# Optimization experiments

Hardware: AMD Instinct MI355X
Metric: run time of the kernel (lower is better)

## Reference

```python
import jax, jax.numpy as jnp
import numpy as np

MIN_NORM = 1e-15

# ---- Poincare-ball (c=1) Mobius algebra, matching geoopt pmath ----

def expmap0(u):
    n = jnp.maximum(jnp.linalg.norm(u, axis=-1, keepdims=True), MIN_NORM)
    return jnp.tanh(n) * u / n

def mobius_add(x, y):
    x2 = jnp.sum(x * x, -1, keepdims=True)
    y2 = jnp.sum(y * y, -1, keepdims=True)
    xy = jnp.sum(x * y, -1, keepdims=True)
    num = (1 + 2 * xy + y2) * x + (1 - x2) * y
    den = 1 + 2 * xy + x2 * y2
    return num / jnp.maximum(den, MIN_NORM)

def mobius_matvec(M, x):
    # M: [H, D, D], x: [B, H, D] -> [B, H, D]  (one matvec per ball)
    x_norm = jnp.maximum(jnp.linalg.norm(x, axis=-1, keepdims=True), MIN_NORM)
    mx = jnp.einsum('hij,bhj->bhi', M, x)
    mx_norm = jnp.maximum(jnp.linalg.norm(mx, axis=-1, keepdims=True), MIN_NORM)
    scale = jnp.tanh(mx_norm / x_norm * jnp.arctanh(jnp.minimum(x_norm, 1 - 1e-7)))
    res = scale * mx / mx_norm
    zero_mx = jnp.all(mx == 0, axis=-1, keepdims=True)
    return jnp.where(zero_mx, jnp.zeros_like(res), res)

def hyper_rnn(x_seq, W, U, b):
    # x_seq: [B, S, H, D] -> encodings [B, S, H, D]
    B, S, H, D = x_seq.shape
    h0 = jnp.zeros((B, H, D), x_seq.dtype)
    def step(h, x_t):
        wh = mobius_matvec(W, h)
        ux = mobius_matvec(U, x_t)
        h_new = mobius_add(mobius_add(wh, ux), b)
        return h_new, h_new
    _, out = jax.lax.scan(step, h0, jnp.swapaxes(x_seq, 0, 1))
    return jnp.swapaxes(out, 0, 1)

def poinc_dist_all_labels(enc, label_embed):
    # enc: [B,S,H,D], label_embed: [L,H,D] -> dist [B,S,L,H]
    # dist(x,y) = arccosh(1 + 2||x-y||^2 / ((1-||x||^2)(1-||y||^2)))  (c=1)
    a = jnp.sum(enc * enc, -1)                 # [B,S,H]
    lb = jnp.sum(label_embed * label_embed, -1)  # [L,H]
    dot = jnp.einsum('bshd,lhd->bslh', enc, label_embed)  # [B,S,L,H]
    c2 = jnp.maximum(a[:, :, None, :] + lb[None, None, :, :] - 2 * dot, 0.0)
    denom = (1 - a)[:, :, None, :] * (1 - lb)[None, None, :, :]
    arg = 1 + 2 * c2 / jnp.maximum(denom, MIN_NORM)
    return jnp.arccosh(jnp.maximum(arg, 1 + 1e-7))

def setup_inputs() -> dict:
    key = jax.random.key(0)
    ks = jax.random.split(key, 10)
    B, S, V, L, H, D = 32, 256, 30000, 1024, 4, 64
    k = 1.0 / np.sqrt(D)
    x = jax.random.randint(ks[0], (B, S), 0, V, dtype=jnp.int64) if jax.config.jax_enable_x64 else jax.random.randint(ks[0], (B, S), 0, V, dtype=jnp.int32)
    word_embed = expmap0(0.05 * jax.random.normal(ks[1], (V, H, D), jnp.float32))
    label_embed = expmap0(0.05 * jax.random.normal(ks[2], (L, H, D), jnp.float32))
    W = jax.random.uniform(ks[3], (H, D, D), jnp.float32, -k, k)
    U = jax.random.uniform(ks[4], (H, D, D), jnp.float32, -k, k)
    b = expmap0(0.01 * jax.random.normal(ks[5], (H, D), jnp.float32))
    k1 = 1.0 / np.sqrt(S)
    w1 = jax.random.uniform(ks[6], (S // 2, S), jnp.float32, -k1, k1)
    b1 = jax.random.uniform(ks[7], (S // 2,), jnp.float32, -k1, k1)
    k2 = 1.0 / np.sqrt(S // 2)
    w2 = jax.random.uniform(ks[8], (1, S // 2), jnp.float32, -k2, k2)
    b2 = jax.random.uniform(ks[9], (1,), jnp.float32, -k2, k2)
    return {"x": x, "word_embed": word_embed, "label_embed": label_embed,
            "W": W, "U": U, "b": b, "w1": w1, "b1": b1, "w2": w2, "b2": b2}

def reference(x, word_embed, label_embed, W, U, b, w1, b1, w2, b2):
    we = word_embed[x]                         # [B,S,H,D]
    enc = hyper_rnn(we, W, U, b)               # [B,S,H,D]
    dist = poinc_dist_all_labels(enc, label_embed)  # [B,S,L,H]
    interaction = jnp.transpose(dist.sum(-1), (0, 2, 1))  # [B,L,S]
    h1 = jax.nn.relu(jnp.einsum('bls,fs->blf', interaction, w1) + b1)
    out = (jnp.einsum('blf,of->blo', h1, w2) + b2).squeeze(-1)  # [B,L]
    return out
```

## Files before the change

### kernel.cpp

```cpp
#include <hip/hip_runtime.h>
#include <math.h>

#define MIN_NORM 1e-15f


__device__ __forceinline__ float frcp(float x){ return __builtin_amdgcn_rcpf(x); }
__device__ __forceinline__ float fsqrt(float x){ return __builtin_amdgcn_sqrtf(x); }
__device__ __forceinline__ float fast_atanh(float x){
  return 0.5f * __logf((1.f + x) * frcp(1.f - x));
}
__device__ __forceinline__ float fast_tanh(float y){
  float e = __expf(-2.f * y);
  return (1.f - e) * frcp(1.f + e);
}
__device__ __forceinline__ float rdlane(float v, int l){
  return __int_as_float(__builtin_amdgcn_readlane(__float_as_int(v), l));
}

#define DPPADD(v, ctrl) \
  v += __int_as_float(__builtin_amdgcn_update_dpp(0, __float_as_int(v), ctrl, 0xf, 0xf, false));

__device__ __forceinline__ float wred_b(float v){
  DPPADD(v,0x111) DPPADD(v,0x112) DPPADD(v,0x114) DPPADD(v,0x118)
  DPPADD(v,0x142) DPPADD(v,0x143)
  return __int_as_float(__builtin_amdgcn_readlane(__float_as_int(v), 63));
}
__device__ __forceinline__ void wred3_b(float& v0, float& v1, float& v2){
  DPPADD(v0,0x111) DPPADD(v1,0x111) DPPADD(v2,0x111)
  DPPADD(v0,0x112) DPPADD(v1,0x112) DPPADD(v2,0x112)
  DPPADD(v0,0x114) DPPADD(v1,0x114) DPPADD(v2,0x114)
  DPPADD(v0,0x118) DPPADD(v1,0x118) DPPADD(v2,0x118)
  DPPADD(v0,0x142) DPPADD(v1,0x142) DPPADD(v2,0x142)
  DPPADD(v0,0x143) DPPADD(v1,0x143) DPPADD(v2,0x143)
  v0 = __int_as_float(__builtin_amdgcn_readlane(__float_as_int(v0), 63));
  v1 = __int_as_float(__builtin_amdgcn_readlane(__float_as_int(v1), 63));
  v2 = __int_as_float(__builtin_amdgcn_readlane(__float_as_int(v2), 63));
}

__device__ __forceinline__ float wred(float v){
#pragma unroll
  for(int o=32;o;o>>=1) v += __shfl_xor(v, o, 64);
  return v;
}

#define LDS_FENCE() asm volatile("s_waitcnt lgkmcnt(0)" ::: "memory")

#define MATVEC64(RES, WROW, HSARR) {                                     \
  float a0=0.f,a1=0.f,a2=0.f,a3=0.f,a4=0.f,a5=0.f,a6=0.f,a7=0.f;         \
  _Pragma("unroll")                                                      \
  for(int j=0;j<64;j+=8){                                                \
    float4 h4 = *(const float4*)(&(HSARR)[j]);                           \
    float4 h5 = *(const float4*)(&(HSARR)[j+4]);                         \
    a0 = fmaf((WROW)[j  ], h4.x, a0); a1 = fmaf((WROW)[j+1], h4.y, a1);  \
    a2 = fmaf((WROW)[j+2], h4.z, a2); a3 = fmaf((WROW)[j+3], h4.w, a3);  \
    a4 = fmaf((WROW)[j+4], h5.x, a4); a5 = fmaf((WROW)[j+5], h5.y, a5);  \
    a6 = fmaf((WROW)[j+6], h5.z, a6); a7 = fmaf((WROW)[j+7], h5.w, a7);  \
  }                                                                      \
  RES = ((a0+a1)+(a2+a3)) + ((a4+a5)+(a6+a7));                           \
}

#define MATVEC_RL(RES, WROW, MV) {                                       \
  float a0=0.f,a1=0.f,a2=0.f,a3=0.f,a4=0.f,a5=0.f,a6=0.f,a7=0.f;         \
  _Pragma("unroll")                                                      \
  for(int j=0;j<64;j+=8){                                                \
    a0 = fmaf(rdlane(MV,j  ), (WROW)[j  ], a0);                          \
    a1 = fmaf(rdlane(MV,j+1), (WROW)[j+1], a1);                          \
    a2 = fmaf(rdlane(MV,j+2), (WROW)[j+2], a2);                          \
    a3 = fmaf(rdlane(MV,j+3), (WROW)[j+3], a3);                          \
    a4 = fmaf(rdlane(MV,j+4), (WROW)[j+4], a4);                          \
    a5 = fmaf(rdlane(MV,j+5), (WROW)[j+5], a5);                          \
    a6 = fmaf(rdlane(MV,j+6), (WROW)[j+6], a6);                          \
    a7 = fmaf(rdlane(MV,j+7), (WROW)[j+7], a7);                          \
  }                                                                      \
  RES = ((a0+a1)+(a2+a3)) + ((a4+a5)+(a6+a7));                           \
}

__global__ __launch_bounds__(256) void k_ux(const int* __restrict__ x,
    const float* __restrict__ wemb, const float* __restrict__ U,
    const float* __restrict__ Wm, const float* __restrict__ bvec,
    float* __restrict__ ux, float* __restrict__ wux,
    float* __restrict__ uxn2, float* __restrict__ uxb){
  __shared__ __align__(16) float xs[4][64];
  const int wv = threadIdx.x >> 6, lane = threadIdx.x & 63;
  const int bid = blockIdx.x*4 + wv;
  const int h = bid & 3;
  const int bs = bid >> 2;
  const int v = x[bs];
  float xi = wemb[(size_t)v*256 + h*64 + lane];
  const float bi = bvec[h*64 + lane];
  xs[wv][lane] = xi;
  LDS_FENCE();
  float mx; MATVEC64(mx, U + h*4096 + lane*64, xs[wv]);
  float t0 = xi*xi, t1 = mx*mx, t2 = mx*bi;
  wred3_b(t0, t1, t2);
  float xn  = fmaxf(fsqrt(t0), MIN_NORM);
  float mxn = fmaxf(fsqrt(t1), MIN_NORM);
  float scale = fast_tanh(mxn*frcp(xn) * fast_atanh(fminf(xn, 1.f-1e-7f)));
  float sm = scale * frcp(mxn);
  float uxv = sm * mx;
  ux[(size_t)bid*64 + lane] = uxv;
  if(lane==0){
    uxn2[bid] = (t1 > 0.f) ? scale*scale : 0.f;
    uxb[bid]  = sm * t2;
  }
  xs[wv][lane] = uxv;
  LDS_FENCE();
  float wuv; MATVEC64(wuv, Wm + h*4096 + lane*64, xs[wv]);
  wux[(size_t)bid*64 + lane] = wuv;
}

#define RNN_STEP(S, USLOT, WUSLOT, Y2V, UBV) {                           \
  const float U_ = USLOT, WU_ = WUSLOT;                                  \
  const float Y2_ = (Y2V), UB_ = (UBV);                                  \
  if((S) < 254){                                   \
    USLOT  = uxp  [(size_t)((S)+2)*256 + lane];                          \
    WUSLOT = wuxp [(size_t)((S)+2)*256 + lane];                          \
  }                                                                      \
  float p0 = m*m, p1 = m*U_, p2 = m*bi;                                  \
  wred3_b(p0, p1, p2);                                                   \
  float r_; MATVEC_RL(r_, wrow, m);           \
  float xn  = fmaxf(fsqrt(hh), MIN_NORM);                                \
  float mxn = fmaxf(fsqrt(p0), MIN_NORM);                                \
  float at  = fast_atanh(fminf(xn, 1.f-1e-7f));                          \
  float scale = fast_tanh(mxn*frcp(xn)*at);                              \
  float sm  = scale*frcp(mxn);                                           \
  float wx2 = (p0 > 0.f) ? scale*scale : 0.f;                            \
  float xy  = sm*p1;                                                     \
  float A   = 1.f + 2.f*xy + Y2_;                                        \
  float Bc  = 1.f - wx2;                                                 \
  float iden = frcp(fmaxf(1.f + 2.f*xy + wx2*Y2_, MIN_NORM));            \
  float c1 = A*sm*iden, c2 = Bc*iden;                                    \
  float zz = (A*A*wx2 + 2.f*A*Bc*xy + Bc*Bc*Y2_)*iden*iden;              \
  float zb = (A*sm*p2 + Bc*UB_)*iden;                                    \
  float A2 = 1.f + 2.f*zb + bn2v;                                        \
  float B2 = 1.f - zz;                                                   \
  float iden2 = frcp(fmaxf(1.f + 2.f*zb + zz*bn2v, MIN_NORM));           \
  float e  = A2*iden2, ga = B2*iden2;                                    \
  float al = e*c1, be = e*c2;                                            \
  encp[(size_t)(S)*256 + lane] = fmaf(al, m, fmaf(be, U_, ga*bi));       \
  hh = fmaxf(e*e*zz + 2.f*e*ga*zb + ga*ga*bn2v, 0.f);                    \
  m  = fmaf(al, r_, fmaf(be, WU_, ga*wb));                               \
}

#define RNN_BLOCK(BLK, Y2R, UBR)                                         \
  for(int i=0;i<64;i+=2){                                                \
    RNN_STEP((BLK)*64+i,   uA, wuA, rdlane(Y2R, i),   rdlane(UBR, i));   \
    RNN_STEP((BLK)*64+i+1, uB, wuB, rdlane(Y2R, i+1), rdlane(UBR, i+1)); \
  }

__global__ __launch_bounds__(64) void k_rnn(const float* __restrict__ W,
    const float* __restrict__ bvec, const float* __restrict__ ux,
    const float* __restrict__ wux, const float* __restrict__ uxn2,
    const float* __restrict__ uxb, float* __restrict__ enc){
  const int b = blockIdx.x >> 2, h = blockIdx.x & 3;
  const int lane = threadIdx.x;
  float wrow[64];
  const float* Wp = W + h*4096 + lane*64;
#pragma unroll
  for(int j=0;j<64;j+=4){
    float4 w4 = *(const float4*)(Wp + j);
    wrow[j]=w4.x; wrow[j+1]=w4.y; wrow[j+2]=w4.z; wrow[j+3]=w4.w;
  }
  const float bi = bvec[h*64 + lane];
  const float bn2v = wred_b(bi*bi);
  float wb; MATVEC_RL(wb, wrow, bi);
  const float* uxp   = ux   + (size_t)b*65536 + h*64;
  const float* wuxp  = wux  + (size_t)b*65536 + h*64;
  const float* uxn2p = uxn2 + (size_t)b*1024  + h;
  const float* uxbp  = uxb  + (size_t)b*1024  + h;
  float* encp        = enc  + (size_t)b*65536 + h*64;
  float y2r0 = uxn2p[(      lane)*4], ubr0 = uxbp[(      lane)*4];
  float y2r1 = uxn2p[( 64 + lane)*4], ubr1 = uxbp[( 64 + lane)*4];
  float y2r2 = uxn2p[(128 + lane)*4], ubr2 = uxbp[(128 + lane)*4];
  float y2r3 = uxn2p[(192 + lane)*4], ubr3 = uxbp[(192 + lane)*4];
  float uA  = uxp[lane],         wuA = wuxp[lane];
  float uB  = uxp[256+lane],     wuB = wuxp[256+lane];
  float m = 0.f, hh = 0.f;
  RNN_BLOCK(0, y2r0, ubr0)
  RNN_BLOCK(1, y2r1, ubr1)
  RNN_BLOCK(2, y2r2, ubr2)
  RNN_BLOCK(3, y2r3, ubr3)
}

__global__ __launch_bounds__(256) void k_norm2(const float* __restrict__ src,
    float* __restrict__ dst, int nrows){
  const int row = blockIdx.x*4 + (threadIdx.x>>6);
  const int lane = threadIdx.x & 63;
  if(row >= nrows) return;
  float v = src[(size_t)row*64 + lane];
  float n2 = wred(v*v);
  if(lane==0) dst[row] = n2;
}

__device__ __forceinline__ float pdist(float dot, float a, float lb){
  float c2  = fmaxf(a + lb - 2.f*dot, 0.f);
  float iden = frcp(fmaxf((1.f-a)*(1.f-lb), MIN_NORM));
  float y   = fmaxf(2.f*c2*iden, 1e-7f);
  return __logf(1.f + y + fsqrt(y*(2.f+y)));
}

#define LP 68
__global__ __launch_bounds__(256) void k_dist(const float* __restrict__ enc,
    const float* __restrict__ lab, const float* __restrict__ an,
    const float* __restrict__ lbn, float* __restrict__ inter){
  __shared__ __align__(16) float eT[4*16*LP];
  __shared__ __align__(16) float lT[4*16*LP];
  const int bs0 = blockIdx.x*64, l0 = blockIdx.y*64;
  const int t = threadIdx.x;
  const int tr = t>>4, tc = t&15;
  const int ldr = t>>2, ldp = t&3;
  float acc[4][4][4];
#pragma unroll
  for(int h=0;h<4;h++)
#pragma unroll
    for(int i=0;i<4;i++)
#pragma unroll
      for(int j=0;j<4;j++) acc[h][i][j]=0.f;

  for(int c=0;c<4;c++){
    if(c) __syncthreads();
#pragma unroll
    for(int h=0;h<4;h++){
      float4 ev = *(const float4*)&enc[(size_t)(bs0+ldr)*256 + h*64 + c*16 + ldp*4];
      float4 lv = *(const float4*)&lab[(size_t)(l0 +ldr)*256 + h*64 + c*16 + ldp*4];
      int base = (h*16 + ldp*4)*LP + ldr;
      eT[base     ] = ev.x; eT[base+  LP] = ev.y; eT[base+2*LP] = ev.z; eT[base+3*LP] = ev.w;
      lT[base     ] = lv.x; lT[base+  LP] = lv.y; lT[base+2*LP] = lv.z; lT[base+3*LP] = lv.w;
    }
    __syncthreads();
#pragma unroll
    for(int dd=0;dd<16;dd++){
#pragma unroll
      for(int h=0;h<4;h++){
        float4 e4 = *(const float4*)&eT[(h*16+dd)*LP + tr*4];
        float4 l4 = *(const float4*)&lT[(h*16+dd)*LP + tc*4];
        float ee[4] = {e4.x,e4.y,e4.z,e4.w};
        float ll[4] = {l4.x,l4.y,l4.z,l4.w};
#pragma unroll
        for(int i=0;i<4;i++)
#pragma unroll
          for(int j=0;j<4;j++)
            acc[h][i][j] = fmaf(ee[i], ll[j], acc[h][i][j]);
      }
    }
  }
  const int b = bs0 >> 8;
#pragma unroll
  for(int i=0;i<4;i++){
    const int bs = bs0 + tr*4 + i;
    const int s  = bs & 255;
    float4 ah = *(const float4*)&an[(size_t)bs*4];
#pragma unroll
    for(int j=0;j<4;j++){
      const int l = l0 + tc*4 + j;
      float4 lb = *(const float4*)&lbn[(size_t)l*4];
      float d = pdist(acc[0][i][j], ah.x, lb.x)
              + pdist(acc[1][i][j], ah.y, lb.y)
              + pdist(acc[2][i][j], ah.z, lb.z)
              + pdist(acc[3][i][j], ah.w, lb.w);
      inter[((size_t)b*1024 + l)*256 + s] = d;
    }
  }
}

__global__ __launch_bounds__(256) void k_mlp(const float* __restrict__ inter,
    const float* __restrict__ w1, const float* __restrict__ b1,
    const float* __restrict__ w2, const float* __restrict__ b2,
    float* __restrict__ out){
  __shared__ __align__(16) float rows[32*256];
  __shared__ float part[4][16];
  const int b  = blockIdx.x >> 5;
  const int l0 = (blockIdx.x & 31)*32;
  const int t = threadIdx.x;
  const float* ip = inter + ((size_t)b*1024 + l0)*256;
#pragma unroll
  for(int k=0;k<8;k++){
    int idx = k*1024 + t*4;
    *(float4*)&rows[idx] = *(const float4*)&ip[idx];
  }
  __syncthreads();
  const int f = t & 127, g = t >> 7;
  float acc[16];
#pragma unroll
  for(int li=0;li<16;li++) acc[li]=0.f;
  const float* wp = w1 + (size_t)f*256;
  for(int s=0;s<256;s+=4){
    float4 w4 = *(const float4*)&wp[s];
#pragma unroll
    for(int li=0;li<16;li++){
      float4 r4 = *(const float4*)&rows[(g*16+li)*256 + s];
      acc[li] = fmaf(r4.w, w4.w, fmaf(r4.z, w4.z, fmaf(r4.y, w4.y, fmaf(r4.x, w4.x, acc[li]))));
    }
  }
  const float bb1 = b1[f], ww2 = w2[f];
  const int wave = t>>6, lane = t&63;
#pragma unroll
  for(int li=0;li<16;li++){
    float vv = fmaxf(acc[li] + bb1, 0.f) * ww2;
    vv = wred(vv);
    if(lane==0) part[wave][li] = vv;
  }
  __syncthreads();
  if(t < 32){
    int g2 = t>>4, li = t&15;
    out[(size_t)b*1024 + l0 + g2*16 + li] = part[2*g2][li] + part[2*g2+1][li] + b2[0];
  }
}

extern "C" void kernel_launch(void* const* d_in, const int* in_sizes, int n_in,
                              void* d_out, int out_size, void* d_ws, size_t ws_size,
                              hipStream_t stream){
  const int*   x    = (const int*)d_in[0];
  const float* wemb = (const float*)d_in[1];
  const float* lab  = (const float*)d_in[2];
  const float* W    = (const float*)d_in[3];
  const float* U    = (const float*)d_in[4];
  const float* bv   = (const float*)d_in[5];
  const float* w1   = (const float*)d_in[6];
  const float* b1   = (const float*)d_in[7];
  const float* w2   = (const float*)d_in[8];
  const float* b2   = (const float*)d_in[9];
  float* out = (float*)d_out;

  float* ws    = (float*)d_ws;
  float* enc   = ws;
  float* an    = enc + 2097152;
  float* lbn   = an  + 32768;
  float* ux    = lbn + 4096;
  float* uxn2  = ux  + 2097152;
  float* uxb   = uxn2 + 32768;
  float* wux   = uxb + 32768;
  float* inter = lbn + 4096;

  k_ux   <<<8192, 256, 0, stream>>>(x, wemb, U, W, bv, ux, wux, uxn2, uxb);
  k_norm2<<<1024, 256, 0, stream>>>(lab, lbn, 4096);
  k_rnn  <<<128,   64, 0, stream>>>(W, bv, ux, wux, uxn2, uxb, enc);
  k_norm2<<<8192, 256, 0, stream>>>(enc, an, 32768);
  dim3 g3(128, 16);
  k_dist <<<g3,   256, 0, stream>>>(enc, lab, an, lbn, inter);
  k_mlp  <<<1024, 256, 0, stream>>>(inter, w1, b1, w2, b2, out);
}
```

Measured before the change: 469.0 us.

## Precompute W·U product and batch input projections per wave with register-resident rows

```diff
diff --git a/kernel.cpp b/kernel.cpp
--- a/kernel.cpp
+++ b/kernel.cpp
@@ -44,20 +44,6 @@
 }
 
 #define LDS_FENCE() asm volatile("s_waitcnt lgkmcnt(0)" ::: "memory")
-
-#define MATVEC64(RES, WROW, HSARR) {                                     \
-  float a0=0.f,a1=0.f,a2=0.f,a3=0.f,a4=0.f,a5=0.f,a6=0.f,a7=0.f;         \
-  _Pragma("unroll")                                                      \
-  for(int j=0;j<64;j+=8){                                                \
-    float4 h4 = *(const float4*)(&(HSARR)[j]);                           \
-    float4 h5 = *(const float4*)(&(HSARR)[j+4]);                         \
-    a0 = fmaf((WROW)[j  ], h4.x, a0); a1 = fmaf((WROW)[j+1], h4.y, a1);  \
-    a2 = fmaf((WROW)[j+2], h4.z, a2); a3 = fmaf((WROW)[j+3], h4.w, a3);  \
-    a4 = fmaf((WROW)[j+4], h5.x, a4); a5 = fmaf((WROW)[j+5], h5.y, a5);  \
-    a6 = fmaf((WROW)[j+6], h5.z, a6); a7 = fmaf((WROW)[j+7], h5.w, a7);  \
-  }                                                                      \
-  RES = ((a0+a1)+(a2+a3)) + ((a4+a5)+(a6+a7));                           \
-}
 
 #define MATVEC_RL(RES, WROW, MV) {                                       \
   float a0=0.f,a1=0.f,a2=0.f,a3=0.f,a4=0.f,a5=0.f,a6=0.f,a7=0.f;         \
@@ -75,38 +61,91 @@
   RES = ((a0+a1)+(a2+a3)) + ((a4+a5)+(a6+a7));                           \
 }
 
+#define MATVEC_RL2(R1, W1, R2, W2, MV) {                                 \
+  float a0=0.f,a1=0.f,a2=0.f,a3=0.f, c0=0.f,c1=0.f,c2=0.f,c3=0.f;        \
+  _Pragma("unroll")                                                      \
+  for(int j=0;j<64;j+=4){                                                \
+    float s0 = rdlane(MV,j  ), s1 = rdlane(MV,j+1);                      \
+    float s2 = rdlane(MV,j+2), s3 = rdlane(MV,j+3);                      \
+    a0 = fmaf(s0,(W1)[j  ],a0); c0 = fmaf(s0,(W2)[j  ],c0);              \
+    a1 = fmaf(s1,(W1)[j+1],a1); c1 = fmaf(s1,(W2)[j+1],c1);              \
+    a2 = fmaf(s2,(W1)[j+2],a2); c2 = fmaf(s2,(W2)[j+2],c2);              \
+    a3 = fmaf(s3,(W1)[j+3],a3); c3 = fmaf(s3,(W2)[j+3],c3);              \
+  }                                                                      \
+  R1 = (a0+a1)+(a2+a3); R2 = (c0+c1)+(c2+c3);                            \
+}
+
+__global__ __launch_bounds__(256) void k_wu(const float* __restrict__ W,
+    const float* __restrict__ U, float* __restrict__ WU){
+  __shared__ float Ws[64*65];
+  __shared__ float Us[64*64];
+  const int h = blockIdx.x;
+  const int t = threadIdx.x;
+#pragma unroll
+  for(int k=0;k<16;k+=4){
+    float4 w4 = *(const float4*)&W[h*4096 + t*16 + k];
+    Ws[(t>>2)*65 + (t&3)*16 + k  ] = w4.x; Ws[(t>>2)*65 + (t&3)*16 + k+1] = w4.y;
+    Ws[(t>>2)*65 + (t&3)*16 + k+2] = w4.z; Ws[(t>>2)*65 + (t&3)*16 + k+3] = w4.w;
+    *(float4*)&Us[t*16 + k] = *(const float4*)&U[h*4096 + t*16 + k];
+  }
+  __syncthreads();
+  const int i = t>>2, j0 = (t&3)*16;
+  float acc[16];
+#pragma unroll
+  for(int j=0;j<16;j++) acc[j]=0.f;
+  for(int k=0;k<64;k++){
+    float w = Ws[i*65+k];
+#pragma unroll
+    for(int j=0;j<16;j++) acc[j] = fmaf(w, Us[k*64+j0+j], acc[j]);
+  }
+#pragma unroll
+  for(int j=0;j<16;j+=4)
+    *(float4*)&WU[h*4096 + i*64 + j0 + j] = make_float4(acc[j],acc[j+1],acc[j+2],acc[j+3]);
+}
+
 __global__ __launch_bounds__(256) void k_ux(const int* __restrict__ x,
     const float* __restrict__ wemb, const float* __restrict__ U,
-    const float* __restrict__ Wm, const float* __restrict__ bvec,
+    const float* __restrict__ WU, const float* __restrict__ bvec,
     float* __restrict__ ux, float* __restrict__ wux,
     float* __restrict__ uxn2, float* __restrict__ uxb){
-  __shared__ __align__(16) float xs[4][64];
   const int wv = threadIdx.x >> 6, lane = threadIdx.x & 63;
-  const int bid = blockIdx.x*4 + wv;
-  const int h = bid & 3;
-  const int bs = bid >> 2;
-  const int v = x[bs];
-  float xi = wemb[(size_t)v*256 + h*64 + lane];
+  const int h = blockIdx.x & 3;
+  const int bs0 = (blockIdx.x >> 2)*32 + wv*8;
+  float urow[64], wurow[64];
+  const float* Up  = U  + h*4096 + lane*64;
+  const float* WUp = WU + h*4096 + lane*64;
+#pragma unroll
+  for(int j=0;j<64;j+=4){
+    float4 a = *(const float4*)(Up + j);
+    urow[j]=a.x; urow[j+1]=a.y; urow[j+2]=a.z; urow[j+3]=a.w;
+    float4 c = *(const float4*)(WUp + j);
+    wurow[j]=c.x; wurow[j+1]=c.y; wurow[j+2]=c.z; wurow[j+3]=c.w;
+  }
   const float bi = bvec[h*64 + lane];
-  xs[wv][lane] = xi;
-  LDS_FENCE();
-  float mx; MATVEC64(mx, U + h*4096 + lane*64, xs[wv]);
-  float t0 = xi*xi, t1 = mx*mx, t2 = mx*bi;
-  wred3_b(t0, t1, t2);
-  float xn  = fmaxf(fsqrt(t0), MIN_NORM);
-  float mxn = fmaxf(fsqrt(t1), MIN_NORM);
-  float scale = fast_tanh(mxn*frcp(xn) * fast_atanh(fminf(xn, 1.f-1e-7f)));
-  float sm = scale * frcp(mxn);
-  float uxv = sm * mx;
-  ux[(size_t)bid*64 + lane] = uxv;
-  if(lane==0){
-    uxn2[bid] = (t1 > 0.f) ? scale*scale : 0.f;
-    uxb[bid]  = sm * t2;
-  }
-  xs[wv][lane] = uxv;
-  LDS_FENCE();
-  float wuv; MATVEC64(wuv, Wm + h*4096 + lane*64, xs[wv]);
-  wux[(size_t)bid*64 + lane] = wuv;
+  int vv[8];
+#pragma unroll
+  for(int k=0;k<8;k++) vv[k] = x[bs0+k];
+  float xv[8];
+#pragma unroll
+  for(int k=0;k<8;k++) xv[k] = wemb[(size_t)vv[k]*256 + h*64 + lane];
+#pragma unroll 2
+  for(int k=0;k<8;k++){
+    float mx, wmx;
+    MATVEC_RL2(mx, urow, wmx, wurow, xv[k]);
+    float t0 = xv[k]*xv[k], t1 = mx*mx, t2 = mx*bi;
+    wred3_b(t0, t1, t2);
+    float xn  = fmaxf(fsqrt(t0), MIN_NORM);
+    float mxn = fmaxf(fsqrt(t1), MIN_NORM);
+    float scale = fast_tanh(mxn*frcp(xn) * fast_atanh(fminf(xn, 1.f-1e-7f)));
+    float sm = scale * frcp(mxn);
+    const int bid = (bs0+k)*4 + h;
+    ux [(size_t)bid*64 + lane] = sm * mx;
+    wux[(size_t)bid*64 + lane] = sm * wmx;
+    if(lane==0){
+      uxn2[bid] = (t1 > 0.f) ? scale*scale : 0.f;
+      uxb[bid]  = sm * t2;
+    }
+  }
 }
 
 #define RNN_STEP(S, USLOT, WUSLOT, Y2V, UBV) {                           \
@@ -330,9 +369,11 @@
   float* uxn2  = ux  + 2097152;
   float* uxb   = uxn2 + 32768;
   float* wux   = uxb + 32768;
+  float* WU    = wux + 2097152;
   float* inter = lbn + 4096;
 
-  k_ux   <<<8192, 256, 0, stream>>>(x, wemb, U, W, bv, ux, wux, uxn2, uxb);
+  k_wu   <<<4,    256, 0, stream>>>(W, U, WU);
+  k_ux   <<<1024, 256, 0, stream>>>(x, wemb, U, WU, bv, ux, wux, uxn2, uxb);
   k_norm2<<<1024, 256, 0, stream>>>(lab, lbn, 4096);
   k_rnn  <<<128,   64, 0, stream>>>(W, bv, ux, wux, uxn2, uxb, enc);
   k_norm2<<<8192, 256, 0, stream>>>(enc, an, 32768);
```

After: 384.6 us. 1.22x faster.
